# Kernel optimization log

Measured on AMD Instinct MI355X. Metric: run time of the kernel, lower is better.

## Reference

```python
import jax, jax.numpy as jnp
import numpy as np

B, S, C, HD = 2, 1024, 1024, 64
H = C // HD  # 16 heads
E = 4
EPS = 1e-5


def _ln(x, g, b):
    m = jnp.mean(x, axis=-1, keepdims=True)
    v = jnp.mean(jnp.square(x - m), axis=-1, keepdims=True)
    return (x - m) / jnp.sqrt(v + EPS) * g + b


def setup_inputs() -> dict:
    key = jax.random.key(0)
    ks = jax.random.split(key, 16)
    s = 0.02
    return {
        "fwd_x": jax.random.normal(ks[0], (B, S + 1, C), jnp.float32),
        "bwd_x": jax.random.normal(ks[1], (B, S + 1, C), jnp.float32),
        "pos_embed": jax.random.normal(ks[2], (S, HD), jnp.float32) * 0.01,
        "ln1_g": jnp.ones((C,), jnp.float32),
        "ln1_b": jnp.zeros((C,), jnp.float32),
        "Wq": jax.random.normal(ks[3], (C, C), jnp.float32) * s,
        "bq": jnp.zeros((C,), jnp.float32),
        "Wk": jax.random.normal(ks[4], (C, C), jnp.float32) * s,
        "bk": jnp.zeros((C,), jnp.float32),
        "Wv": jax.random.normal(ks[5], (C, C), jnp.float32) * s,
        "bv": jnp.zeros((C,), jnp.float32),
        "Wo": jax.random.normal(ks[6], (C, C), jnp.float32) * s,
        "bo": jnp.zeros((C,), jnp.float32),
        "ln2_g": jnp.ones((C,), jnp.float32),
        "ln2_b": jnp.zeros((C,), jnp.float32),
        "mlp_g": jnp.ones((C,), jnp.float32),
        "mlp_b": jnp.zeros((C,), jnp.float32),
        "W1": jax.random.normal(ks[7], (C, E * C), jnp.float32) * s,
        "b1": jnp.zeros((E * C,), jnp.float32),
        "W2": jax.random.normal(ks[8], (E * C, C), jnp.float32) * s,
        "b2": jnp.zeros((C,), jnp.float32),
    }


def reference(fwd_x, bwd_x, pos_embed, ln1_g, ln1_b, Wq, bq, Wk, bk, Wv, bv,
              Wo, bo, ln2_g, ln2_b, mlp_g, mlp_b, W1, b1, W2, b2):
    f = fwd_x[:, :-1, :]   # [B, S, C]
    r = bwd_x[:, 1:, :]    # [B, S, C]
    comb = (f + r) * np.float32(1.0 / np.sqrt(2.0))

    all_embed = jnp.concatenate([f, r], axis=1)       # [B, 2S, C]
    cx = _ln(comb, ln1_g, ln1_b)
    ae = _ln(all_embed, ln1_g, ln1_b)

    q = (cx @ Wq + bq).reshape(B, S, H, HD)
    k = (ae @ Wk + bk).reshape(B, 2 * S, H, HD)
    v = (ae @ Wv + bv).reshape(B, 2 * S, H, HD)

    pos2 = jnp.concatenate([pos_embed, pos_embed], axis=0)  # [2S, HD]
    k = k + pos2[None, :, None, :]
    q = (q + pos_embed[None, :, None, :]) * np.float32(1.0 / np.sqrt(HD))

    logits = jnp.einsum('bqhd,bkhd->bhqk', q, k)      # [B, H, S, 2S]

    qi = jnp.arange(S)[:, None]
    ki = jnp.arange(S)[None, :]
    l2r = ki <= qi   # causal (keys up to and incl. q) on first half
    r2l = ki >= qi   # anti-causal on second half
    mask = jnp.concatenate([l2r, r2l], axis=-1)        # [S, 2S]

    neg = jnp.finfo(logits.dtype).min
    attn = jax.nn.softmax(jnp.where(mask[None, None], logits, neg), axis=-1)

    o = jnp.einsum('bhqk,bkhd->bqhd', attn, v).reshape(B, S, C)
    o = o @ Wo + bo

    x = comb + o
    h = _ln(_ln(x, ln2_g, ln2_b), mlp_g, mlp_b)
    m = jax.nn.gelu(h @ W1 + b1, approximate=False) @ W2 + b2
    return x + m
```

## Files before the change

### kernel.cpp

```cpp
#include <hip/hip_runtime.h>
#include <hip/hip_bf16.h>
#include <cstdint>

#define DI __device__ __forceinline__

typedef unsigned short u16;
typedef __bf16 bf16x8 __attribute__((ext_vector_type(8)));
typedef float f32x4 __attribute__((ext_vector_type(4)));

constexpr int Bc  = 2;
constexpr int Sc  = 1024;
constexpr int Cc  = 1024;
constexpr int Hc  = 16;
constexpr int HDc = 64;
constexpr int S2c = 2048;
constexpr int ECc = 4096;
constexpr int BSc  = Bc * Sc;
constexpr int BS2c = Bc * S2c;

constexpr int EPI_KV = 0, EPI_Q = 1, EPI_O = 3, EPI_GELU = 4, EPI_FINAL = 5, EPI_PART = 6;

DI u16 f2b(float f) {
  __hip_bfloat16 h = __float2bfloat16(f);
  u16 u;
  __builtin_memcpy(&u, &h, 2);
  return u;
}

DI u16 f2b_fast(float f) {
  uint32_t u;
  __builtin_memcpy(&u, &f, 4);
  return (u16)((u + 0x8000u) >> 16);
}

DI void glds16(const void* g, void* l) {
  auto* lp = reinterpret_cast<__attribute__((address_space(3))) uint32_t*>(
      reinterpret_cast<uintptr_t>(l));
  __builtin_amdgcn_global_load_lds(
      reinterpret_cast<const __attribute__((address_space(1))) uint32_t*>(
          reinterpret_cast<uintptr_t>(g)),
      lp, 16, 0, 0);
}

DI f32x4 mfma16(bf16x8 a, bf16x8 b, f32x4 c) {
  return __builtin_amdgcn_mfma_f32_16x16x32_bf16(a, b, c, 0, 0, 0);
}

__global__ __launch_bounds__(256) void transpose4_kernel(const float* __restrict__ Wq,
                                                         const float* __restrict__ Wk,
                                                         const float* __restrict__ Wv,
                                                         const float* __restrict__ Wo,
                                                         u16* __restrict__ WqT,
                                                         u16* __restrict__ WkvT,
                                                         u16* __restrict__ WoT) {
  __shared__ float tile[32][33];
  const int z = blockIdx.z;
  const float* W = (z == 0) ? Wq : (z == 1) ? Wk : (z == 2) ? Wv : Wo;
  u16* WT = (z == 0) ? WqT : (z == 1) ? WkvT : (z == 2) ? (WkvT + (size_t)Cc * Cc) : WoT;
  const int bx = blockIdx.x, by = blockIdx.y;
  const int tx = threadIdx.x, ty = threadIdx.y;
  const int c = bx * 32 + tx;
#pragma unroll
  for (int i = ty; i < 32; i += 8) tile[i][tx] = W[(size_t)(by * 32 + i) * Cc + c];
  __syncthreads();
#pragma unroll
  for (int i = ty; i < 32; i += 8)
    WT[(size_t)(bx * 32 + i) * Cc + by * 32 + tx] = f2b(tile[tx][i]);
}

__global__ __launch_bounds__(256) void transpose_kernel(const float* __restrict__ W,
                                                        u16* __restrict__ WT, int R, int Cn) {
  __shared__ float tile[32][33];
  const int bx = blockIdx.x, by = blockIdx.y;
  const int tx = threadIdx.x, ty = threadIdx.y;
  const int c = bx * 32 + tx;
#pragma unroll
  for (int i = ty; i < 32; i += 8) tile[i][tx] = W[(size_t)(by * 32 + i) * Cn + c];
  __syncthreads();
#pragma unroll
  for (int i = ty; i < 32; i += 8)
    WT[(size_t)(bx * 32 + i) * R + by * 32 + tx] = f2b(tile[tx][i]);
}

__global__ __launch_bounds__(256) void prep_ln_kernel(
    const float* __restrict__ fwd, const float* __restrict__ bwd, const float* __restrict__ g,
    const float* __restrict__ be, float* __restrict__ comb, u16* __restrict__ cx,
    u16* __restrict__ ae) {
  __shared__ float red[2][4];
  const int row = blockIdx.x, tid = threadIdx.x;
  const int c = tid * 4;
  float4 x;
  u16* dst;
  if (row < BSc) {
    const int b = row >> 10, s = row & (Sc - 1);
    const float4 f = *(const float4*)(fwd + ((size_t)(b * (Sc + 1) + s)) * Cc + c);
    const float4 r = *(const float4*)(bwd + ((size_t)(b * (Sc + 1) + s + 1)) * Cc + c);
    const float k = 0.70710678118654752f;
    x.x = (f.x + r.x) * k; x.y = (f.y + r.y) * k;
    x.z = (f.z + r.z) * k; x.w = (f.w + r.w) * k;
    *(float4*)(comb + (size_t)row * Cc + c) = x;
    dst = cx + (size_t)row * Cc;
  } else {
    const int idx = row - BSc;
    const int b = idx >> 11, t = idx & (S2c - 1);
    const float* src = (t < Sc) ? (fwd + ((size_t)(b * (Sc + 1) + t)) * Cc)
                                : (bwd + ((size_t)(b * (Sc + 1) + (t - Sc) + 1)) * Cc);
    x = *(const float4*)(src + c);
    dst = ae + (size_t)idx * Cc;
  }
  float s1 = x.x + x.y + x.z + x.w;
  float s2 = x.x * x.x + x.y * x.y + x.z * x.z + x.w * x.w;
  for (int off = 32; off; off >>= 1) { s1 += __shfl_down(s1, off); s2 += __shfl_down(s2, off); }
  if ((tid & 63) == 0) { red[0][tid >> 6] = s1; red[1][tid >> 6] = s2; }
  __syncthreads();
  s1 = red[0][0] + red[0][1] + red[0][2] + red[0][3];
  s2 = red[1][0] + red[1][1] + red[1][2] + red[1][3];
  const float mean = s1 * (1.0f / Cc);
  const float rstd = rsqrtf(s2 * (1.0f / Cc) - mean * mean + 1e-5f);
  const float4 gv = *(const float4*)(g + c);
  const float4 bv = *(const float4*)(be + c);
  ushort4 o;
  o.x = f2b((x.x - mean) * rstd * gv.x + bv.x);
  o.y = f2b((x.y - mean) * rstd * gv.y + bv.y);
  o.z = f2b((x.z - mean) * rstd * gv.z + bv.z);
  o.w = f2b((x.w - mean) * rstd * gv.w + bv.w);
  *(ushort4*)(dst + c) = o;
}

__global__ __launch_bounds__(256) void ln2_kernel(const float* __restrict__ x,
                                                  const float* __restrict__ g2,
                                                  const float* __restrict__ b2,
                                                  const float* __restrict__ gm,
                                                  const float* __restrict__ bm,
                                                  u16* __restrict__ h) {
  __shared__ float red[2][4];
  const int row = blockIdx.x, tid = threadIdx.x;
  const int c = tid * 4;
  const float4 v = *(const float4*)(x + (size_t)row * Cc + c);
  float s1 = v.x + v.y + v.z + v.w;
  float s2 = v.x * v.x + v.y * v.y + v.z * v.z + v.w * v.w;
  for (int off = 32; off; off >>= 1) { s1 += __shfl_down(s1, off); s2 += __shfl_down(s2, off); }
  if ((tid & 63) == 0) { red[0][tid >> 6] = s1; red[1][tid >> 6] = s2; }
  __syncthreads();
  s1 = red[0][0] + red[0][1] + red[0][2] + red[0][3];
  s2 = red[1][0] + red[1][1] + red[1][2] + red[1][3];
  float mean = s1 * (1.0f / Cc);
  float rstd = rsqrtf(s2 * (1.0f / Cc) - mean * mean + 1e-5f);
  const float4 ga = *(const float4*)(g2 + c);
  const float4 ba = *(const float4*)(b2 + c);
  const float t0 = (v.x - mean) * rstd * ga.x + ba.x;
  const float t1 = (v.y - mean) * rstd * ga.y + ba.y;
  const float t2 = (v.z - mean) * rstd * ga.z + ba.z;
  const float t3 = (v.w - mean) * rstd * ga.w + ba.w;
  s1 = t0 + t1 + t2 + t3;
  s2 = t0 * t0 + t1 * t1 + t2 * t2 + t3 * t3;
  for (int off = 32; off; off >>= 1) { s1 += __shfl_down(s1, off); s2 += __shfl_down(s2, off); }
  __syncthreads();
  if ((tid & 63) == 0) { red[0][tid >> 6] = s1; red[1][tid >> 6] = s2; }
  __syncthreads();
  s1 = red[0][0] + red[0][1] + red[0][2] + red[0][3];
  s2 = red[1][0] + red[1][1] + red[1][2] + red[1][3];
  mean = s1 * (1.0f / Cc);
  rstd = rsqrtf(s2 * (1.0f / Cc) - mean * mean + 1e-5f);
  const float4 gb = *(const float4*)(gm + c);
  const float4 bb = *(const float4*)(bm + c);
  ushort4 o;
  o.x = f2b((t0 - mean) * rstd * gb.x + bb.x);
  o.y = f2b((t1 - mean) * rstd * gb.y + bb.y);
  o.z = f2b((t2 - mean) * rstd * gb.z + bb.z);
  o.w = f2b((t3 - mean) * rstd * gb.w + bb.w);
  *(ushort4*)(h + (size_t)row * Cc + c) = o;
}

template <int EPI, int SK>
__global__ __launch_bounds__(256) void gemm_kernel(
    const u16* __restrict__ A, const u16* __restrict__ BT, const float* __restrict__ bias,
    const float* __restrict__ bias2, const float* __restrict__ pos,
    u16* __restrict__ outb, u16* __restrict__ out2, float* __restrict__ pbuf,
    int M, int N, int K) {
  __shared__ u16 Asm[2][128 * 32];
  __shared__ u16 Bsm[2][128 * 32];
  const int tid = threadIdx.x;
  const int w = tid >> 6, lane = tid & 63, quad = lane >> 4, r16 = lane & 15;
  const int bm = blockIdx.y * 128, bn = blockIdx.x * 128;
  const int wm = (w & 1) * 64, wn = (w >> 1) * 64;
  const int Ks = K / SK, kb0 = blockIdx.z * Ks;

  const int srow = lane >> 2, scol = (lane & 3) * 8;
  const u16* aP = A + (size_t)(bm + w * 32 + srow) * K + kb0 + scol;
  const u16* bP = BT + (size_t)(bn + w * 32 + srow) * K + kb0 + scol;
  const size_t rstep = (size_t)16 * K;
  const int l0 = (w * 32) * 32;
  const int l1 = (w * 32 + 16) * 32;

  f32x4 acc[4][4] = {};

  auto STAGE = [&](int buf, int ko) {
    glds16(aP + ko, &Asm[buf][l0]);
    glds16(aP + ko + rstep, &Asm[buf][l1]);
    glds16(bP + ko, &Bsm[buf][l0]);
    glds16(bP + ko + rstep, &Bsm[buf][l1]);
  };
  auto COMPUTE = [&](int buf) {
    bf16x8 af[4], bfr[4];
#pragma unroll
    for (int i = 0; i < 4; i++) {
      af[i] = *reinterpret_cast<const bf16x8*>(&Asm[buf][(wm + i * 16 + r16) * 32 + quad * 8]);
      bfr[i] = *reinterpret_cast<const bf16x8*>(&Bsm[buf][(wn + i * 16 + r16) * 32 + quad * 8]);
    }
#pragma unroll
    for (int mi = 0; mi < 4; mi++)
#pragma unroll
      for (int ni = 0; ni < 4; ni++) acc[mi][ni] = mfma16(af[mi], bfr[ni], acc[mi][ni]);
  };

  const int NT = Ks / 32;
  STAGE(0, 0);
  __syncthreads();
  for (int t = 0; t < NT; t += 2) {
    STAGE(1, (t + 1) * 32);
    COMPUTE(0);
    __syncthreads();
    if (t + 2 < NT) STAGE(0, (t + 2) * 32);
    COMPUTE(1);
    __syncthreads();
  }

#pragma unroll
  for (int mi = 0; mi < 4; mi++) {
#pragma unroll
    for (int ni = 0; ni < 4; ni++) {
      const int col = bn + wn + ni * 16 + r16;
      const int row0 = bm + wm + mi * 16 + quad * 4;
      if constexpr (EPI == EPI_PART) {
        float* pb = pbuf + (size_t)blockIdx.z * M * N;
#pragma unroll
        for (int r = 0; r < 4; r++) pb[(size_t)(row0 + r) * N + col] = acc[mi][ni][r];
      } else if constexpr (EPI == EPI_KV) {
        if (col < Cc) {
#pragma unroll
          for (int r = 0; r < 4; r++) {
            const int row = row0 + r;
            const int key = row & (S2c - 1);
            const float y =
                acc[mi][ni][r] + bias[col] + pos[(key & (Sc - 1)) * HDc + (col & 63)];
            outb[(size_t)row * Cc + col] = f2b(y);
          }
        } else {
          const int c2 = col - Cc;
          const int h = c2 >> 6, d = c2 & 63;
          const int b = row0 >> 11, key0 = row0 & (S2c - 1);
          const float bb = bias2[c2];
          ushort4 pk;
          pk.x = f2b(acc[mi][ni][0] + bb);
          pk.y = f2b(acc[mi][ni][1] + bb);
          pk.z = f2b(acc[mi][ni][2] + bb);
          pk.w = f2b(acc[mi][ni][3] + bb);
          *(ushort4*)&out2[(((size_t)(b * Hc + h) * HDc + d) << 11) + key0] = pk;
        }
      } else {
#pragma unroll
        for (int r = 0; r < 4; r++) {
          const float y = acc[mi][ni][r] + bias[col];
          outb[(size_t)(row0 + r) * N + col] =
              f2b(0.5f * y * (1.0f + erff(y * 0.70710678118654752f)));
        }
      }
    }
  }
}

template <int EPI, int SK>
__global__ __launch_bounds__(256) void reduce_kernel(const float* __restrict__ pbuf,
                                                     const float* __restrict__ bias,
                                                     const float* __restrict__ pos,
                                                     const float* __restrict__ addsrc,
                                                     u16* __restrict__ outb,
                                                     float* __restrict__ outf, int M, int N) {
  const size_t flat = ((size_t)blockIdx.x * 256 + threadIdx.x) * 4;
  const int row = (int)(flat / N), col = (int)(flat % N);
  const size_t MN = (size_t)M * N;
  float4 s = *(const float4*)(pbuf + flat);
#pragma unroll
  for (int z = 1; z < SK; z++) {
    const float4 v = *(const float4*)(pbuf + z * MN + flat);
    s.x += v.x; s.y += v.y; s.z += v.z; s.w += v.w;
  }
  const float4 bv = *(const float4*)(bias + col);
  s.x += bv.x; s.y += bv.y; s.z += bv.z; s.w += bv.w;
  if constexpr (EPI == EPI_Q) {
    const int sq = row & (Sc - 1), d = col & 63;
    const float4 pv = *(const float4*)(pos + sq * HDc + d);
    constexpr float sc = 0.180336880111120426f;
    ushort4 o;
    o.x = f2b((s.x + pv.x) * sc);
    o.y = f2b((s.y + pv.y) * sc);
    o.z = f2b((s.z + pv.z) * sc);
    o.w = f2b((s.w + pv.w) * sc);
    *(ushort4*)(outb + flat) = o;
  } else {
    const float4 av = *(const float4*)(addsrc + flat);
    float4 o;
    o.x = s.x + av.x; o.y = s.y + av.y; o.z = s.z + av.z; o.w = s.w + av.w;
    *(float4*)(outf + flat) = o;
  }
}

__global__ __launch_bounds__(256) void attn_part_kernel(const u16* __restrict__ qb,
                                                        const u16* __restrict__ kb,
                                                        const u16* __restrict__ vT,
                                                        float* __restrict__ o_part,
                                                        float* __restrict__ l_part) {
  const int bh = blockIdx.x;
  const int qt = blockIdx.y;
  const int half = blockIdx.z;
  const int b = bh >> 4, head = bh & 15;
  const int tid = threadIdx.x;
  const int w = tid >> 6, lane = tid & 63, quad = lane >> 4, r16 = lane & 15;

  __shared__ u16 Kt[2][64 * 32];
  __shared__ u16 Vt[2][64 * 32];
  __shared__ u16 Ps[4][16 * 68];
  u16* ps = Ps[w];

  const int q0 = qt * 64;
  const int qw = q0 + w * 16;

  bf16x8 aq[2];
  {
    const u16* qp = qb + ((size_t)((b * Sc + qw + r16) * Hc + head)) * HDc + quad * 8;
    aq[0] = *(const bf16x8*)qp;
    aq[1] = *(const bf16x8*)(qp + 32);
  }

  const size_t krow = (size_t)Hc * HDc;
  const u16* kbase = kb + ((size_t)b * S2c * Hc + head) * HDc;
  const u16* vbase = vT + ((size_t)(b * Hc + head)) * HDc * S2c;

  const int srow = w * 16 + (lane >> 2);
  const int scol = (lane & 3) * 8;
  u16* kD0 = &Kt[0][w * 16 * 32];
  u16* kD1 = &Kt[1][w * 16 * 32];
  u16* vD0 = &Vt[0][w * 16 * 32];
  u16* vD1 = &Vt[1][w * 16 * 32];
  const u16* kS = kbase + (size_t)srow * krow + scol;
  const u16* vS = vbase + (size_t)srow * S2c + scol;

  f32x4 o_acc[4] = {};
  float lsum[4] = {};

  const int n = (half == 0) ? (qt + 1) : (16 - qt);
  const int kb0 = (half == 0) ? 0 : Sc + qt * 64;

  for (int j = 0; j < n; j++) {
    const int k0 = kb0 + j * 64;
    glds16(kS + (size_t)k0 * krow, kD0);
    glds16(kS + (size_t)k0 * krow + 32, kD1);
    glds16(vS + k0, vD0);
    glds16(vS + k0 + 32, vD1);
    __syncthreads();

    f32x4 sacc[4] = {};
#pragma unroll
    for (int ks = 0; ks < 2; ks++)
#pragma unroll
      for (int ni = 0; ni < 4; ni++) {
        const bf16x8 bk = *(const bf16x8*)&Kt[ks][(ni * 16 + r16) * 32 + quad * 8];
        sacc[ni] = mfma16(aq[ks], bk, sacc[ni]);
      }

    const int mode = (half == 0) ? ((j == n - 1) ? 1 : 0) : ((j == 0) ? 2 : 0);
#pragma unroll
    for (int r = 0; r < 4; r++) {
      const int qrow = qw + quad * 4 + r;
#pragma unroll
      for (int ni = 0; ni < 4; ni++) {
        float s = sacc[ni][r];
        if (mode == 1) { const int key = k0 + ni * 16 + r16; if (key > qrow) s = -128.0f; }
        else if (mode == 2) { const int key = k0 - Sc + ni * 16 + r16; if (key < qrow) s = -128.0f; }
        const float pe = __builtin_amdgcn_exp2f(s);
        lsum[r] += pe;
        ps[(quad * 4 + r) * 68 + ni * 16 + r16] = f2b_fast(pe);
      }
    }

#pragma unroll
    for (int ks = 0; ks < 2; ks++) {
      const bf16x8 ap = *(const bf16x8*)(&ps[r16 * 68 + ks * 32 + quad * 8]);
#pragma unroll
      for (int ni = 0; ni < 4; ni++) {
        const bf16x8 bv_ = *(const bf16x8*)&Vt[ks][(ni * 16 + r16) * 32 + quad * 8];
        o_acc[ni] = mfma16(ap, bv_, o_acc[ni]);
      }
    }
    __syncthreads();
  }

#pragma unroll
  for (int r = 0; r < 4; r++) {
    float l = lsum[r];
    l += __shfl_xor(l, 1);
    l += __shfl_xor(l, 2);
    l += __shfl_xor(l, 4);
    l += __shfl_xor(l, 8);
    lsum[r] = l;
  }

  const size_t rowbase = (((size_t)half * Bc + b) * Hc + head) * Sc + qw;
  float* ob = o_part + rowbase * HDc;
#pragma unroll
  for (int r = 0; r < 4; r++) {
    const int rl = quad * 4 + r;
#pragma unroll
    for (int ni = 0; ni < 4; ni++) ob[(size_t)rl * HDc + ni * 16 + r16] = o_acc[ni][r];
    if (r16 == 0) l_part[rowbase + rl] = lsum[r];
  }
}

__global__ __launch_bounds__(256) void attn_norm_kernel(const float* __restrict__ o_part,
                                                        const float* __restrict__ l_part,
                                                        u16* __restrict__ ob) {
  constexpr size_t HS = (size_t)Bc * Hc * Sc * HDc;
  constexpr size_t HL = (size_t)Bc * Hc * Sc;
  const int flat = blockIdx.x * 256 + threadIdx.x;
  const int row = flat >> 4, d0 = (flat & 15) * 4;
  const int q = row & (Sc - 1), h = (row >> 10) & 15, b = row >> 14;
  const float4 o0 = *(const float4*)(o_part + (size_t)row * HDc + d0);
  const float4 o1 = *(const float4*)(o_part + HS + (size_t)row * HDc + d0);
  const float rl = 1.0f / (l_part[row] + l_part[HL + row]);
  ushort4 o;
  o.x = f2b((o0.x + o1.x) * rl);
  o.y = f2b((o0.y + o1.y) * rl);
  o.z = f2b((o0.z + o1.z) * rl);
  o.w = f2b((o0.w + o1.w) * rl);
  *(ushort4*)(ob + ((size_t)((b * Sc + q) * Hc + h)) * HDc + d0) = o;
}

extern "C" void kernel_launch(void* const* d_in, const int* in_sizes, int n_in, void* d_out,
                              int out_size, void* d_ws, size_t ws_size, hipStream_t stream) {
  const float* fwd = (const float*)d_in[0];
  const float* bwd = (const float*)d_in[1];
  const float* pos = (const float*)d_in[2];
  const float* ln1g = (const float*)d_in[3];
  const float* ln1b = (const float*)d_in[4];
  const float* Wq = (const float*)d_in[5];
  const float* bq = (const float*)d_in[6];
  const float* Wk = (const float*)d_in[7];
  const float* bk = (const float*)d_in[8];
  const float* Wv = (const float*)d_in[9];
  const float* bv = (const float*)d_in[10];
  const float* Wo = (const float*)d_in[11];
  const float* bo = (const float*)d_in[12];
  const float* ln2g = (const float*)d_in[13];
  const float* ln2b = (const float*)d_in[14];
  const float* mlpg = (const float*)d_in[15];
  const float* mlpb = (const float*)d_in[16];
  const float* W1 = (const float*)d_in[17];
  const float* b1 = (const float*)d_in[18];
  const float* W2 = (const float*)d_in[19];
  const float* b2 = (const float*)d_in[20];

  char* p = (char*)d_ws;
  auto alloc = [&](size_t bytes) -> char* {
    char* r = p;
    p += (bytes + 255) & ~(size_t)255;
    return r;
  };
  float* comb = (float*)alloc((size_t)BSc * Cc * 4);
  float* xbuf = (float*)alloc((size_t)BSc * Cc * 4);
  u16* cx = (u16*)alloc((size_t)BSc * Cc * 2);
  u16* ae = (u16*)alloc((size_t)BS2c * Cc * 2);
  u16* qbuf = (u16*)alloc((size_t)BSc * Cc * 2);
  u16* kbuf = (u16*)alloc((size_t)BS2c * Cc * 2);
  u16* vTb = (u16*)alloc((size_t)BS2c * Cc * 2);
  u16* obuf = (u16*)alloc((size_t)BSc * Cc * 2);
  u16* hb = (u16*)alloc((size_t)BSc * Cc * 2);
  char* big = alloc((size_t)2 * BSc * Hc * HDc * 4 > (size_t)BSc * ECc * 2
                        ? (size_t)2 * BSc * Hc * HDc * 4
                        : (size_t)BSc * ECc * 2);
  float* o_part = (float*)big;
  u16* midb = (u16*)big;
  float* l_part = (float*)alloc((size_t)2 * Bc * Hc * Sc * 4);
  float* pbuf = (float*)alloc((size_t)4 * BSc * Cc * 4);
  u16* WqT = (u16*)alloc((size_t)Cc * Cc * 2);
  u16* WkvT = (u16*)alloc((size_t)2 * Cc * Cc * 2);
  u16* WoT = (u16*)alloc((size_t)Cc * Cc * 2);
  u16* W1T = (u16*)alloc((size_t)ECc * Cc * 2);
  u16* W2T = (u16*)alloc((size_t)Cc * ECc * 2);

  const dim3 tb(32, 8);
  transpose4_kernel<<<dim3(32, 32, 4), tb, 0, stream>>>(Wq, Wk, Wv, Wo, WqT, WkvT, WoT);
  transpose_kernel<<<dim3(128, 32), tb, 0, stream>>>(W1, W1T, Cc, ECc);
  transpose_kernel<<<dim3(32, 128), tb, 0, stream>>>(W2, W2T, ECc, Cc);

  prep_ln_kernel<<<BSc + BS2c, 256, 0, stream>>>(fwd, bwd, ln1g, ln1b, comb, cx, ae);

  gemm_kernel<EPI_PART, 4><<<dim3(Cc / 128, BSc / 128, 4), 256, 0, stream>>>(
      cx, WqT, nullptr, nullptr, nullptr, nullptr, nullptr, pbuf, BSc, Cc, Cc);
  reduce_kernel<EPI_Q, 4><<<(BSc * Cc / 4) / 256, 256, 0, stream>>>(
      pbuf, bq, pos, nullptr, qbuf, nullptr, BSc, Cc);

  gemm_kernel<EPI_KV, 1><<<dim3(2 * Cc / 128, BS2c / 128, 1), 256, 0, stream>>>(
      ae, WkvT, bk, bv, pos, kbuf, vTb, nullptr, BS2c, 2 * Cc, Cc);

  attn_part_kernel<<<dim3(Bc * Hc, Sc / 64, 2), 256, 0, stream>>>(qbuf, kbuf, vTb, o_part,
                                                                  l_part);
  attn_norm_kernel<<<(BSc * Hc * HDc / 4) / 256, 256, 0, stream>>>(o_part, l_part, obuf);

  gemm_kernel<EPI_PART, 4><<<dim3(Cc / 128, BSc / 128, 4), 256, 0, stream>>>(
      obuf, WoT, nullptr, nullptr, nullptr, nullptr, nullptr, pbuf, BSc, Cc, Cc);
  reduce_kernel<EPI_O, 4><<<(BSc * Cc / 4) / 256, 256, 0, stream>>>(
      pbuf, bo, nullptr, comb, nullptr, xbuf, BSc, Cc);

  ln2_kernel<<<BSc, 256, 0, stream>>>(xbuf, ln2g, ln2b, mlpg, mlpb, hb);

  gemm_kernel<EPI_GELU, 1><<<dim3(ECc / 128, BSc / 128, 1), 256, 0, stream>>>(
      hb, W1T, b1, nullptr, nullptr, midb, nullptr, nullptr, BSc, ECc, Cc);

  gemm_kernel<EPI_PART, 4><<<dim3(Cc / 128, BSc / 128, 4), 256, 0, stream>>>(
      midb, W2T, nullptr, nullptr, nullptr, nullptr, nullptr, pbuf, BSc, Cc, ECc);
  reduce_kernel<EPI_FINAL, 4><<<(BSc * Cc / 4) / 256, 256, 0, stream>>>(
      pbuf, b2, nullptr, xbuf, nullptr, (float*)d_out, BSc, Cc);
}
```

Measured before the change: 347.5 us.

## Deepen GEMM LDS pipeline to four stages with explicit vmcnt waits

Replaces the double-buffered GEMM main loop with a four-buffer ring that keeps two tile loads in flight. Explicit s_waitcnt vmcnt counts and raw s_barrier calls with sched_barrier replace __syncthreads. The aim is to hide global-to-LDS latency behind the MFMA work. It doubles LDS use to 64KB per block, which can lower occupancy. The loop assumes NT is a multiple of 4, and the barrier placement has to be correct or buffer reuse will race.

```diff
diff --git a/kernel.cpp b/kernel.cpp
--- a/kernel.cpp
+++ b/kernel.cpp
@@ -45,6 +45,17 @@
 DI f32x4 mfma16(bf16x8 a, bf16x8 b, f32x4 c) {
   return __builtin_amdgcn_mfma_f32_16x16x32_bf16(a, b, c, 0, 0, 0);
 }
+
+#define PIPE_WAIT(N)                                            \
+  do {                                                          \
+    asm volatile("s_waitcnt vmcnt(" #N ")" ::: "memory");       \
+    __builtin_amdgcn_sched_barrier(0);                          \
+  } while (0)
+#define PIPE_BAR()                                              \
+  do {                                                          \
+    __builtin_amdgcn_s_barrier();                               \
+    __builtin_amdgcn_sched_barrier(0);                          \
+  } while (0)
 
 __global__ __launch_bounds__(256) void transpose4_kernel(const float* __restrict__ Wq,
                                                          const float* __restrict__ Wk,
@@ -178,8 +189,8 @@
     const float* __restrict__ bias2, const float* __restrict__ pos,
     u16* __restrict__ outb, u16* __restrict__ out2, float* __restrict__ pbuf,
     int M, int N, int K) {
-  __shared__ u16 Asm[2][128 * 32];
-  __shared__ u16 Bsm[2][128 * 32];
+  __shared__ u16 A0s[128 * 32], A1s[128 * 32], A2s[128 * 32], A3s[128 * 32];
+  __shared__ u16 B0s[128 * 32], B1s[128 * 32], B2s[128 * 32], B3s[128 * 32];
   const int tid = threadIdx.x;
   const int w = tid >> 6, lane = tid & 63, quad = lane >> 4, r16 = lane & 15;
   const int bm = blockIdx.y * 128, bn = blockIdx.x * 128;
@@ -195,18 +206,19 @@
 
   f32x4 acc[4][4] = {};
 
-  auto STAGE = [&](int buf, int ko) {
-    glds16(aP + ko, &Asm[buf][l0]);
-    glds16(aP + ko + rstep, &Asm[buf][l1]);
-    glds16(bP + ko, &Bsm[buf][l0]);
-    glds16(bP + ko + rstep, &Bsm[buf][l1]);
+  auto STAGE = [&](u16* Ad, u16* Bd, int t) {
+    const int ko = t * 32;
+    glds16(aP + ko, Ad + l0);
+    glds16(aP + ko + rstep, Ad + l1);
+    glds16(bP + ko, Bd + l0);
+    glds16(bP + ko + rstep, Bd + l1);
   };
-  auto COMPUTE = [&](int buf) {
+  auto COMPUTE = [&](const u16* As, const u16* Bs) {
     bf16x8 af[4], bfr[4];
 #pragma unroll
     for (int i = 0; i < 4; i++) {
-      af[i] = *reinterpret_cast<const bf16x8*>(&Asm[buf][(wm + i * 16 + r16) * 32 + quad * 8]);
-      bfr[i] = *reinterpret_cast<const bf16x8*>(&Bsm[buf][(wn + i * 16 + r16) * 32 + quad * 8]);
+      af[i] = *reinterpret_cast<const bf16x8*>(&As[(wm + i * 16 + r16) * 32 + quad * 8]);
+      bfr[i] = *reinterpret_cast<const bf16x8*>(&Bs[(wn + i * 16 + r16) * 32 + quad * 8]);
     }
 #pragma unroll
     for (int mi = 0; mi < 4; mi++)
@@ -215,15 +227,29 @@
   };
 
   const int NT = Ks / 32;
-  STAGE(0, 0);
-  __syncthreads();
-  for (int t = 0; t < NT; t += 2) {
-    STAGE(1, (t + 1) * 32);
-    COMPUTE(0);
-    __syncthreads();
-    if (t + 2 < NT) STAGE(0, (t + 2) * 32);
-    COMPUTE(1);
-    __syncthreads();
+  STAGE(A0s, B0s, 0);
+  STAGE(A1s, B1s, 1);
+  for (int t = 0; t < NT; t += 4) {
+    if (t + 2 < NT) { STAGE(A2s, B2s, t + 2); PIPE_WAIT(8); }
+    else if (t + 1 < NT) PIPE_WAIT(4);
+    else PIPE_WAIT(0);
+    PIPE_BAR();
+    COMPUTE(A0s, B0s);
+    if (t + 3 < NT) { STAGE(A3s, B3s, t + 3); PIPE_WAIT(8); }
+    else if (t + 2 < NT) PIPE_WAIT(4);
+    else PIPE_WAIT(0);
+    PIPE_BAR();
+    COMPUTE(A1s, B1s);
+    if (t + 4 < NT) { STAGE(A0s, B0s, t + 4); PIPE_WAIT(8); }
+    else if (t + 3 < NT) PIPE_WAIT(4);
+    else PIPE_WAIT(0);
+    PIPE_BAR();
+    COMPUTE(A2s, B2s);
+    if (t + 5 < NT) { STAGE(A1s, B1s, t + 5); PIPE_WAIT(8); }
+    else if (t + 4 < NT) PIPE_WAIT(4);
+    else PIPE_WAIT(0);
+    PIPE_BAR();
+    COMPUTE(A3s, B3s);
   }
 
 #pragma unroll
```

Measured after the change: 339.4 us. 1.02x faster.
